# Optimization experiments

Hardware: AMD Instinct MI355X
Metric: run time of the kernel (lower is better)

The kernel has to match this reference:

```python
import jax, jax.numpy as jnp
import numpy as np

N = 100000   # num_nodes
E = 1600000  # num_edges
IN, HID, OUT = 128, 128, 64
BN_EPS = 1e-5


def setup_inputs() -> dict:
    key = jax.random.key(0)
    ks = jax.random.split(key, 8)
    x = jax.random.normal(ks[0], (N, IN), jnp.float32)
    edge_index = jax.random.randint(ks[1], (2, E), 0, N)
    edge_weight = jax.random.uniform(ks[2], (E,), jnp.float32)
    W1 = jax.random.normal(ks[3], (IN, HID), jnp.float32) / np.sqrt(IN)
    b1 = jnp.zeros((HID,), jnp.float32)
    gamma = jnp.ones((HID,), jnp.float32)
    beta = jnp.zeros((HID,), jnp.float32)
    W2 = jax.random.normal(ks[4], (HID, OUT), jnp.float32) / np.sqrt(HID)
    b2 = jnp.zeros((OUT,), jnp.float32)
    return {"x": x, "edge_index": edge_index, "edge_weight": edge_weight,
            "W1": W1, "b1": b1, "gamma": gamma, "beta": beta, "W2": W2, "b2": b2}


def _add_self_loops(edge_index, edge_weight, n):
    loops = jnp.arange(n, dtype=edge_index.dtype)
    row = jnp.concatenate([edge_index[0], loops])
    col = jnp.concatenate([edge_index[1], loops])
    ew = jnp.concatenate([edge_weight, jnp.ones((n,), edge_weight.dtype)])
    return row, col, ew


def _gcn_conv(x, row, col, ew, W, b, n):
    h = x @ W                                           # [n, out]
    deg = jax.ops.segment_sum(ew, col, num_segments=n)  # in-degree (incl. self-loops)
    dinv = jnp.where(deg > 0, jax.lax.rsqrt(jnp.where(deg > 0, deg, 1.0)), 0.0)
    norm = dinv[row] * ew * dinv[col]                   # [E+n]
    msg = h[row] * norm[:, None]                        # gather + scale
    out = jax.ops.segment_sum(msg, col, num_segments=n)  # scatter-add at targets
    return out + b


def reference(x, edge_index, edge_weight, W1, b1, gamma, beta, W2, b2):
    n = x.shape[0]
    row, col, ew = _add_self_loops(edge_index, edge_weight, n)
    h = _gcn_conv(x, row, col, ew, W1, b1, n)
    # BatchNorm1d over nodes (training-mode batch stats, biased variance)
    mu = h.mean(axis=0)
    var = ((h - mu) ** 2).mean(axis=0)
    h = (h - mu) * jax.lax.rsqrt(var + BN_EPS) * gamma + beta
    h = jax.nn.relu(h)
    # dropout is identity at inference
    h = _gcn_conv(h, row, col, ew, W2, b2, n)
    return jax.nn.log_softmax(h, axis=1)  # out_feats > 1 branch
```

## Files before the change

kernel.cpp:

```cpp
#include <hip/hip_runtime.h>
#include <math.h>


typedef unsigned int   uint;
typedef unsigned short ushort;
typedef __bf16 bf16x8 __attribute__((ext_vector_type(8)));
typedef float  f32x4  __attribute__((ext_vector_type(4)));

union U16 { uint4 u; bf16x8 b; };

__device__ __forceinline__ void atomAddF(float* p, float v) {
    __hip_atomic_fetch_add(p, v, __ATOMIC_RELAXED, __HIP_MEMORY_SCOPE_AGENT);
}

__device__ __forceinline__ ushort f2bf(float f) {
    uint u = __float_as_uint(f);
    u += 0x7FFFu + ((u >> 16) & 1u);
    return (ushort)(u >> 16);
}
__device__ __forceinline__ float bf2f(ushort h) {
    return __uint_as_float(((uint)h) << 16);
}
__device__ __forceinline__ uint pack2(float f0, float f1) {
    return (uint)f2bf(f0) | ((uint)f2bf(f1) << 16);
}

__global__ void k_init(int* __restrict__ cnt, float* __restrict__ bn, int n) {
    int i = blockIdx.x * 256 + threadIdx.x;
    if (i < n) cnt[i] = 0;
    if (i < 256) bn[i] = 0.0f;
}

__global__ void k_cnt(const int* __restrict__ col, int* __restrict__ cnt,
                      int* __restrict__ rank, int e) {
    int i = blockIdx.x * 256 + threadIdx.x;
    if (i < e) rank[i] = atomicAdd(&cnt[col[i]], 1);
}


__global__ __launch_bounds__(256)
void k_scanA(const int* __restrict__ cnt, int* __restrict__ bsum, int n) {
    __shared__ int ls[256];
    int base = blockIdx.x * 1024 + threadIdx.x * 4;
    int s = 0;
#pragma unroll
    for (int k = 0; k < 4; ++k) { int i = base + k; if (i < n) s += cnt[i]; }
    ls[threadIdx.x] = s;
    __syncthreads();
    for (int d = 128; d > 0; d >>= 1) {
        if (threadIdx.x < d) ls[threadIdx.x] += ls[threadIdx.x + d];
        __syncthreads();
    }
    if (threadIdx.x == 0) bsum[blockIdx.x] = ls[0];
}

__global__ __launch_bounds__(1024)
void k_scanB(int* __restrict__ bsum, int* __restrict__ ptr, int nblk, int n) {
    __shared__ int ls[1024];
    int t = threadIdx.x;
    int v = (t < nblk) ? bsum[t] : 0;
    ls[t] = v;
    __syncthreads();
    for (int d = 1; d < 1024; d <<= 1) {
        int mine = ls[t];
        int up   = (t >= d) ? ls[t - d] : 0;
        __syncthreads();
        ls[t] = mine + up;
        __syncthreads();
    }
    if (t < nblk) bsum[t] = ls[t] - v;
    if (t == 0) ptr[n] = ls[1023];
}

__global__ __launch_bounds__(256)
void k_scanC(const int* __restrict__ cnt, const int* __restrict__ bsum,
             int* __restrict__ ptr, int n) {
    __shared__ int ls[256];
    int base = blockIdx.x * 1024 + threadIdx.x * 4;
    int v[4];
#pragma unroll
    for (int k = 0; k < 4; ++k) { int i = base + k; v[k] = (i < n) ? cnt[i] : 0; }
    int t = v[0] + v[1] + v[2] + v[3];
    ls[threadIdx.x] = t;
    __syncthreads();
    for (int d = 1; d < 256; d <<= 1) {
        int mine = ls[threadIdx.x];
        int up   = (threadIdx.x >= d) ? ls[threadIdx.x - d] : 0;
        __syncthreads();
        ls[threadIdx.x] = mine + up;
        __syncthreads();
    }
    int off = bsum[blockIdx.x] + ls[threadIdx.x] - t;
    int pf = 0;
#pragma unroll
    for (int k = 0; k < 4; ++k) {
        int i = base + k;
        if (i < n) ptr[i] = off + pf;
        pf += v[k];
    }
}

__global__ void k_fill(const int* __restrict__ row, const int* __restrict__ col,
                       const float* __restrict__ ew, const int* __restrict__ rank,
                       const int* __restrict__ ptr, int2* __restrict__ csr, int e) {
    int i = blockIdx.x * 256 + threadIdx.x;
    if (i < e) {
        int pos = ptr[col[i]] + rank[i];
        int2 pr;
        pr.x = row[i];
        pr.y = __float_as_int(ew[i]);
        csr[pos] = pr;
    }
}

__global__ __launch_bounds__(256)
void k_degsum(const int* __restrict__ ptr, const int2* __restrict__ csr,
              float* __restrict__ dinv, int n) {
    int lane = threadIdx.x & 15;
    int node = (blockIdx.x * 256 + threadIdx.x) >> 4;
    if (node >= n) return;
    int p0 = ptr[node], p1 = ptr[node + 1];
    float s = 0.f;
    for (int j = p0 + lane; j < p1; j += 16) s += __int_as_float(csr[j].y);
#pragma unroll
    for (int off = 8; off > 0; off >>= 1) s += __shfl_xor(s, off, 16);
    if (lane == 0) dinv[node] = rsqrtf(1.0f + s);
}

__global__ void k_wfrag(const float* __restrict__ W, uint4* __restrict__ Wf, int M) {
    int t = blockIdx.x * 256 + threadIdx.x;
    if (t >= M * 16) return;
    int l  = t & 63;
    int ks = (t >> 6) & 3;
    int nt = t >> 8;
    int kbase = ks * 32 + (l >> 4) * 8;
    int colj  = nt * 16 + (l & 15);
    float v[8];
#pragma unroll
    for (int j = 0; j < 8; ++j) v[j] = W[(kbase + j) * M + colj];
    uint4 o;
    o.x = pack2(v[0], v[1]);
    o.y = pack2(v[2], v[3]);
    o.z = pack2(v[4], v[5]);
    o.w = pack2(v[6], v[7]);
    Wf[t] = o;
}

template<int M, bool BN>
__global__ __launch_bounds__(256)
void k_mfma(const void* __restrict__ Xv, const uint4* __restrict__ Wf,
            const float* __restrict__ scale, const float* __restrict__ shift,
            ushort* __restrict__ H, int n)
{
    constexpr int NT = M / 16;
    const int l = threadIdx.x & 63;
    const int w = threadIdx.x >> 6;
    const int rowbase = blockIdx.x * 64 + w * 16;
    const int arow = rowbase + (l & 15);
    const bool rv = arow < n;
    const int koff = (l >> 4) * 8;

    f32x4 acc[NT];
#pragma unroll
    for (int t = 0; t < NT; ++t) acc[t] = (f32x4){0.f, 0.f, 0.f, 0.f};

#pragma unroll
    for (int ks = 0; ks < 4; ++ks) {
        U16 ua;
        if (BN) {
            const ushort* xr = (const ushort*)Xv + (size_t)arow * 128 + koff;
            U16 xa; xa.u = make_uint4(0, 0, 0, 0);
            if (rv) xa.u = *(const uint4*)(xr + ks * 32);
            int k0 = ks * 32 + koff;
            float4 sc0 = *(const float4*)(scale + k0);
            float4 sc1 = *(const float4*)(scale + k0 + 4);
            float4 sh0 = *(const float4*)(shift + k0);
            float4 sh1 = *(const float4*)(shift + k0 + 4);
            float a[8];
            a[0] = fmaxf(0.f, fmaf(bf2f((ushort)(xa.u.x)),       sc0.x, sh0.x));
            a[1] = fmaxf(0.f, fmaf(bf2f((ushort)(xa.u.x >> 16)), sc0.y, sh0.y));
            a[2] = fmaxf(0.f, fmaf(bf2f((ushort)(xa.u.y)),       sc0.z, sh0.z));
            a[3] = fmaxf(0.f, fmaf(bf2f((ushort)(xa.u.y >> 16)), sc0.w, sh0.w));
            a[4] = fmaxf(0.f, fmaf(bf2f((ushort)(xa.u.z)),       sc1.x, sh1.x));
            a[5] = fmaxf(0.f, fmaf(bf2f((ushort)(xa.u.z >> 16)), sc1.y, sh1.y));
            a[6] = fmaxf(0.f, fmaf(bf2f((ushort)(xa.u.w)),       sc1.z, sh1.z));
            a[7] = fmaxf(0.f, fmaf(bf2f((ushort)(xa.u.w >> 16)), sc1.w, sh1.w));
            ua.u.x = pack2(a[0], a[1]);
            ua.u.y = pack2(a[2], a[3]);
            ua.u.z = pack2(a[4], a[5]);
            ua.u.w = pack2(a[6], a[7]);
        } else {
            const float* xr = (const float*)Xv + (size_t)arow * 128 + koff;
            float4 a0 = make_float4(0.f, 0.f, 0.f, 0.f);
            float4 a1 = a0;
            if (rv) {
                a0 = *(const float4*)(xr + ks * 32);
                a1 = *(const float4*)(xr + ks * 32 + 4);
            }
            ua.u.x = pack2(a0.x, a0.y);
            ua.u.y = pack2(a0.z, a0.w);
            ua.u.z = pack2(a1.x, a1.y);
            ua.u.w = pack2(a1.z, a1.w);
        }
#pragma unroll
        for (int nt = 0; nt < NT; ++nt) {
            U16 ub;
            ub.u = Wf[(nt * 4 + ks) * 64 + l];
            acc[nt] = __builtin_amdgcn_mfma_f32_16x16x32_bf16(ua.b, ub.b, acc[nt], 0, 0, 0);
        }
    }

    __shared__ __align__(16) ushort lds[4][16][M + 8];
#pragma unroll
    for (int nt = 0; nt < NT; ++nt)
#pragma unroll
        for (int r = 0; r < 4; ++r)
            lds[w][(l >> 4) * 4 + r][nt * 16 + (l & 15)] = f2bf(acc[nt][r]);
    __syncthreads();

    constexpr int LPR = M / 8;
    constexpr int RPP = 64 / LPR;
#pragma unroll
    for (int it = 0; it < 16 / RPP; ++it) {
        int rl = it * RPP + (l / LPR);
        int gr = rowbase + rl;
        if (gr < n)
            *(uint4*)(H + (size_t)gr * M + (l % LPR) * 8) =
                *(const uint4*)&lds[w][rl][(l % LPR) * 8];
    }
}

__global__ __launch_bounds__(256)
void k_gather1(const int* __restrict__ ptr, const int2* __restrict__ csr,
               const ushort* __restrict__ h, const float* __restrict__ dinv,
               const float* __restrict__ bias, ushort* __restrict__ out, int n)
{
    int lane = threadIdx.x & 15;
    int node = (blockIdx.x * 256 + threadIdx.x) >> 4;
    if (node >= n) return;
    int p0 = ptr[node], p1 = ptr[node + 1];
    float di = dinv[node];
    float s  = di * di;

    U16 hv; hv.u = *(const uint4*)(h + (size_t)node * 128 + lane * 8);
    float4 b0 = *(const float4*)(bias + lane * 8);
    float4 b1v = *(const float4*)(bias + lane * 8 + 4);
    float acc[8];
    acc[0] = fmaf(bf2f((ushort)(hv.u.x)),       s, b0.x);
    acc[1] = fmaf(bf2f((ushort)(hv.u.x >> 16)), s, b0.y);
    acc[2] = fmaf(bf2f((ushort)(hv.u.y)),       s, b0.z);
    acc[3] = fmaf(bf2f((ushort)(hv.u.y >> 16)), s, b0.w);
    acc[4] = fmaf(bf2f((ushort)(hv.u.z)),       s, b1v.x);
    acc[5] = fmaf(bf2f((ushort)(hv.u.z >> 16)), s, b1v.y);
    acc[6] = fmaf(bf2f((ushort)(hv.u.w)),       s, b1v.z);
    acc[7] = fmaf(bf2f((ushort)(hv.u.w >> 16)), s, b1v.w);

#pragma unroll 4
    for (int j = p0; j < p1; ++j) {
        int2 pr = csr[j];
        float w = __int_as_float(pr.y) * di * dinv[pr.x];
        U16 v; v.u = *(const uint4*)(h + (size_t)pr.x * 128 + lane * 8);
        acc[0] = fmaf(bf2f((ushort)(v.u.x)),       w, acc[0]);
        acc[1] = fmaf(bf2f((ushort)(v.u.x >> 16)), w, acc[1]);
        acc[2] = fmaf(bf2f((ushort)(v.u.y)),       w, acc[2]);
        acc[3] = fmaf(bf2f((ushort)(v.u.y >> 16)), w, acc[3]);
        acc[4] = fmaf(bf2f((ushort)(v.u.z)),       w, acc[4]);
        acc[5] = fmaf(bf2f((ushort)(v.u.z >> 16)), w, acc[5]);
        acc[6] = fmaf(bf2f((ushort)(v.u.w)),       w, acc[6]);
        acc[7] = fmaf(bf2f((ushort)(v.u.w >> 16)), w, acc[7]);
    }

    U16 o;
    o.u.x = pack2(acc[0], acc[1]);
    o.u.y = pack2(acc[2], acc[3]);
    o.u.z = pack2(acc[4], acc[5]);
    o.u.w = pack2(acc[6], acc[7]);
    *(uint4*)(out + (size_t)node * 128 + lane * 8) = o.u;
}

__global__ __launch_bounds__(256)
void k_gather2(const int* __restrict__ ptr, const int2* __restrict__ csr,
               const ushort* __restrict__ h, const float* __restrict__ dinv,
               const float* __restrict__ bias, float* __restrict__ out, int n)
{
    int lane = threadIdx.x & 7;
    int node = (blockIdx.x * 256 + threadIdx.x) >> 3;
    if (node >= n) return;
    int p0 = ptr[node], p1 = ptr[node + 1];
    float di = dinv[node];
    float s  = di * di;

    U16 hv; hv.u = *(const uint4*)(h + (size_t)node * 64 + lane * 8);
    float4 b0 = *(const float4*)(bias + lane * 8);
    float4 b1v = *(const float4*)(bias + lane * 8 + 4);
    float acc[8];
    acc[0] = fmaf(bf2f((ushort)(hv.u.x)),       s, b0.x);
    acc[1] = fmaf(bf2f((ushort)(hv.u.x >> 16)), s, b0.y);
    acc[2] = fmaf(bf2f((ushort)(hv.u.y)),       s, b0.z);
    acc[3] = fmaf(bf2f((ushort)(hv.u.y >> 16)), s, b0.w);
    acc[4] = fmaf(bf2f((ushort)(hv.u.z)),       s, b1v.x);
    acc[5] = fmaf(bf2f((ushort)(hv.u.z >> 16)), s, b1v.y);
    acc[6] = fmaf(bf2f((ushort)(hv.u.w)),       s, b1v.z);
    acc[7] = fmaf(bf2f((ushort)(hv.u.w >> 16)), s, b1v.w);

#pragma unroll 4
    for (int j = p0; j < p1; ++j) {
        int2 pr = csr[j];
        float w = __int_as_float(pr.y) * di * dinv[pr.x];
        U16 v; v.u = *(const uint4*)(h + (size_t)pr.x * 64 + lane * 8);
        acc[0] = fmaf(bf2f((ushort)(v.u.x)),       w, acc[0]);
        acc[1] = fmaf(bf2f((ushort)(v.u.x >> 16)), w, acc[1]);
        acc[2] = fmaf(bf2f((ushort)(v.u.y)),       w, acc[2]);
        acc[3] = fmaf(bf2f((ushort)(v.u.y >> 16)), w, acc[3]);
        acc[4] = fmaf(bf2f((ushort)(v.u.z)),       w, acc[4]);
        acc[5] = fmaf(bf2f((ushort)(v.u.z >> 16)), w, acc[5]);
        acc[6] = fmaf(bf2f((ushort)(v.u.w)),       w, acc[6]);
        acc[7] = fmaf(bf2f((ushort)(v.u.w >> 16)), w, acc[7]);
    }

    float m = acc[0];
#pragma unroll
    for (int k = 1; k < 8; ++k) m = fmaxf(m, acc[k]);
#pragma unroll
    for (int off = 1; off < 8; off <<= 1) m = fmaxf(m, __shfl_xor(m, off, 64));
    float sum = 0.f;
#pragma unroll
    for (int k = 0; k < 8; ++k) sum += expf(acc[k] - m);
#pragma unroll
    for (int off = 1; off < 8; off <<= 1) sum += __shfl_xor(sum, off, 64);
    float lse = m + logf(sum);

    float* orow = out + (size_t)node * 64 + lane * 8;
    *(float4*)(orow)     = make_float4(acc[0] - lse, acc[1] - lse, acc[2] - lse, acc[3] - lse);
    *(float4*)(orow + 4) = make_float4(acc[4] - lse, acc[5] - lse, acc[6] - lse, acc[7] - lse);
}

__global__ __launch_bounds__(256)
void k_bn_stats(const ushort* __restrict__ a, float* __restrict__ sums,
                float* __restrict__ sumsq, int n)
{
    int fp = threadIdx.x & 63;
    int rg = threadIdx.x >> 6;
    float s0 = 0.f, q0 = 0.f, s1 = 0.f, q1 = 0.f;
    for (int r = blockIdx.x * 4 + rg; r < n; r += gridDim.x * 4) {
        uint v = *(const uint*)(a + (size_t)r * 128 + fp * 2);
        float x0 = bf2f((ushort)v), x1 = bf2f((ushort)(v >> 16));
        s0 += x0; q0 += x0 * x0;
        s1 += x1; q1 += x1 * x1;
    }
    __shared__ float l0[256], l1[256], l2[256], l3[256];
    l0[threadIdx.x] = s0; l1[threadIdx.x] = q0;
    l2[threadIdx.x] = s1; l3[threadIdx.x] = q1;
    __syncthreads();
    if (rg == 0) {
        float S0 = l0[fp] + l0[fp + 64] + l0[fp + 128] + l0[fp + 192];
        float Q0 = l1[fp] + l1[fp + 64] + l1[fp + 128] + l1[fp + 192];
        float S1 = l2[fp] + l2[fp + 64] + l2[fp + 128] + l2[fp + 192];
        float Q1 = l3[fp] + l3[fp + 64] + l3[fp + 128] + l3[fp + 192];
        atomAddF(&sums[fp * 2],     S0);
        atomAddF(&sumsq[fp * 2],    Q0);
        atomAddF(&sums[fp * 2 + 1], S1);
        atomAddF(&sumsq[fp * 2 + 1], Q1);
    }
}

__global__ void k_bn_final(const float* __restrict__ bn, const float* __restrict__ gamma,
                           const float* __restrict__ beta, float* __restrict__ scale,
                           float* __restrict__ shift, int n)
{
    int f = threadIdx.x;
    if (f < 128) {
        float inv_n = 1.0f / (float)n;
        float mu  = bn[f] * inv_n;
        float var = bn[128 + f] * inv_n - mu * mu;
        float rstd = rsqrtf(var + 1e-5f);
        float sc = gamma[f] * rstd;
        scale[f] = sc;
        shift[f] = beta[f] - mu * sc;
    }
}

extern "C" void kernel_launch(void* const* d_in, const int* in_sizes, int n_in,
                              void* d_out, int out_size, void* d_ws, size_t ws_size,
                              hipStream_t stream)
{
    const float* x     = (const float*)d_in[0];
    const int*   ei    = (const int*)  d_in[1];
    const float* ew    = (const float*)d_in[2];
    const float* W1    = (const float*)d_in[3];
    const float* b1    = (const float*)d_in[4];
    const float* gamma = (const float*)d_in[5];
    const float* beta  = (const float*)d_in[6];
    const float* W2    = (const float*)d_in[7];
    const float* b2    = (const float*)d_in[8];

    const int n = in_sizes[0] / 128;
    const int e = in_sizes[2];
    const int* row = ei;
    const int* col = ei + e;

    float* ws    = (float*)d_ws;
    size_t off   = 0;
    float* dinv  = ws + off; off += n;
    ushort* h1   = (ushort*)(ws + off); off += (size_t)n * 64;
    ushort* agg1 = (ushort*)(ws + off); off += (size_t)n * 64;
    float* bn    = ws + off; off += 256;
    float* scale = ws + off; off += 128;
    float* shift = ws + off; off += 128;
    int*   cnt   = (int*)(ws + off); off += n;
    int*   ptr   = (int*)(ws + off); off += (size_t)(n + 1);
    int*   bsum  = (int*)(ws + off); off += 1024;
    off = (off + 3) & ~(size_t)3;
    uint4* w1f   = (uint4*)(ws + off); off += 8192;
    uint4* w2f   = (uint4*)(ws + off); off += 4096;
    int2*  csr   = (int2*)(ws + off);
    int*   rank  = (int*)agg1;
    ushort* h2   = h1;
    float* outp  = (float*)d_out;

    const int nb_n = (n + 255) / 256;
    const int nb_e = (e + 255) / 256;
    const int nb_qpn = (n + 15) / 16;
    const int nb_opn = (n + 31) / 32;
    const int nb_mf  = (n + 63) / 64;
    const int nblk_scan = (n + 1023) / 1024;

    k_wfrag<<<8, 256, 0, stream>>>(W1, w1f, 128);
    k_wfrag<<<4, 256, 0, stream>>>(W2, w2f, 64);

    k_init<<<nb_n, 256, 0, stream>>>(cnt, bn, n);
    k_cnt<<<nb_e, 256, 0, stream>>>(col, cnt, rank, e);
    k_scanA<<<nblk_scan, 256, 0, stream>>>(cnt, bsum, n);
    k_scanB<<<1, 1024, 0, stream>>>(bsum, ptr, nblk_scan, n);
    k_scanC<<<nblk_scan, 256, 0, stream>>>(cnt, bsum, ptr, n);
    k_fill<<<nb_e, 256, 0, stream>>>(row, col, ew, rank, ptr, csr, e);
    k_degsum<<<nb_qpn, 256, 0, stream>>>(ptr, csr, dinv, n);

    k_mfma<128, false><<<nb_mf, 256, 0, stream>>>(x, w1f, nullptr, nullptr, h1, n);
    k_gather1<<<nb_qpn, 256, 0, stream>>>(ptr, csr, h1, dinv, b1, agg1, n);

    k_bn_stats<<<256, 256, 0, stream>>>(agg1, bn, bn + 128, n);
    k_bn_final<<<1, 128, 0, stream>>>(bn, gamma, beta, scale, shift, n);

    k_mfma<64, true><<<nb_mf, 256, 0, stream>>>(agg1, w2f, scale, shift, h2, n);
    k_gather2<<<nb_opn, 256, 0, stream>>>(ptr, csr, h2, dinv, b2, outp, n);
}
```

Baseline: 290.0 us.

## Split per-node edge counters into eight sub-counters to reduce atomic contention

Each node's in-degree counter becomes eight sub-counters, chosen by the low bits of the edge index, so atomic increments on a popular target node are spread out. The scan now runs over n*8 interleaved entries, producing a bucketed CSR pointer array that fill, degsum and the gather kernels index with node<<3. The rank buffer moves to its own workspace region instead of aliasing agg1. In exchange the count/scan arrays are eight times larger, and the scan kernels read them with a strided pattern.

```diff
diff --git a/kernel.cpp b/kernel.cpp
--- a/kernel.cpp
+++ b/kernel.cpp
@@ -25,26 +25,30 @@
     return (uint)f2bf(f0) | ((uint)f2bf(f1) << 16);
 }
 
-__global__ void k_init(int* __restrict__ cnt, float* __restrict__ bn, int n) {
+__global__ void k_init(int* __restrict__ cnt, float* __restrict__ bn, int m) {
     int i = blockIdx.x * 256 + threadIdx.x;
-    if (i < n) cnt[i] = 0;
+    if (i < m) cnt[i] = 0;
     if (i < 256) bn[i] = 0.0f;
 }
 
 __global__ void k_cnt(const int* __restrict__ col, int* __restrict__ cnt,
-                      int* __restrict__ rank, int e) {
+                      int* __restrict__ rank, int e, int n) {
     int i = blockIdx.x * 256 + threadIdx.x;
-    if (i < e) rank[i] = atomicAdd(&cnt[col[i]], 1);
-}
-
-
-__global__ __launch_bounds__(256)
-void k_scanA(const int* __restrict__ cnt, int* __restrict__ bsum, int n) {
+    if (i < e) rank[i] = atomicAdd(&cnt[(i & 7) * n + col[i]], 1);
+}
+
+
+__global__ __launch_bounds__(256)
+void k_scanA(const int* __restrict__ cnt, int* __restrict__ bsum,
+             int m, int n) {
     __shared__ int ls[256];
     int base = blockIdx.x * 1024 + threadIdx.x * 4;
     int s = 0;
 #pragma unroll
-    for (int k = 0; k < 4; ++k) { int i = base + k; if (i < n) s += cnt[i]; }
+    for (int k = 0; k < 4; ++k) {
+        int b = base + k;
+        if (b < m) s += cnt[(b & 7) * n + (b >> 3)];
+    }
     ls[threadIdx.x] = s;
     __syncthreads();
     for (int d = 128; d > 0; d >>= 1) {
@@ -55,7 +59,7 @@
 }
 
 __global__ __launch_bounds__(1024)
-void k_scanB(int* __restrict__ bsum, int* __restrict__ ptr, int nblk, int n) {
+void k_scanB(int* __restrict__ bsum, int* __restrict__ ptr, int nblk, int m) {
     __shared__ int ls[1024];
     int t = threadIdx.x;
     int v = (t < nblk) ? bsum[t] : 0;
@@ -69,17 +73,20 @@
         __syncthreads();
     }
     if (t < nblk) bsum[t] = ls[t] - v;
-    if (t == 0) ptr[n] = ls[1023];
+    if (t == 0) ptr[m] = ls[1023];
 }
 
 __global__ __launch_bounds__(256)
 void k_scanC(const int* __restrict__ cnt, const int* __restrict__ bsum,
-             int* __restrict__ ptr, int n) {
+             int* __restrict__ ptr, int m, int n) {
     __shared__ int ls[256];
     int base = blockIdx.x * 1024 + threadIdx.x * 4;
     int v[4];
 #pragma unroll
-    for (int k = 0; k < 4; ++k) { int i = base + k; v[k] = (i < n) ? cnt[i] : 0; }
+    for (int k = 0; k < 4; ++k) {
+        int b = base + k;
+        v[k] = (b < m) ? cnt[(b & 7) * n + (b >> 3)] : 0;
+    }
     int t = v[0] + v[1] + v[2] + v[3];
     ls[threadIdx.x] = t;
     __syncthreads();
@@ -94,8 +101,8 @@
     int pf = 0;
 #pragma unroll
     for (int k = 0; k < 4; ++k) {
-        int i = base + k;
-        if (i < n) ptr[i] = off + pf;
+        int b = base + k;
+        if (b < m) ptr[b] = off + pf;
         pf += v[k];
     }
 }
@@ -105,7 +112,7 @@
                        const int* __restrict__ ptr, int2* __restrict__ csr, int e) {
     int i = blockIdx.x * 256 + threadIdx.x;
     if (i < e) {
-        int pos = ptr[col[i]] + rank[i];
+        int pos = ptr[(col[i] << 3) + (i & 7)] + rank[i];
         int2 pr;
         pr.x = row[i];
         pr.y = __float_as_int(ew[i]);
@@ -119,7 +126,7 @@
     int lane = threadIdx.x & 15;
     int node = (blockIdx.x * 256 + threadIdx.x) >> 4;
     if (node >= n) return;
-    int p0 = ptr[node], p1 = ptr[node + 1];
+    int p0 = ptr[node << 3], p1 = ptr[(node << 3) + 8];
     float s = 0.f;
     for (int j = p0 + lane; j < p1; j += 16) s += __int_as_float(csr[j].y);
 #pragma unroll
@@ -238,7 +245,7 @@
     int lane = threadIdx.x & 15;
     int node = (blockIdx.x * 256 + threadIdx.x) >> 4;
     if (node >= n) return;
-    int p0 = ptr[node], p1 = ptr[node + 1];
+    int p0 = ptr[node << 3], p1 = ptr[(node << 3) + 8];
     float di = dinv[node];
     float s  = di * di;
 
@@ -286,7 +293,7 @@
     int lane = threadIdx.x & 7;
     int node = (blockIdx.x * 256 + threadIdx.x) >> 3;
     if (node >= n) return;
-    int p0 = ptr[node], p1 = ptr[node + 1];
+    int p0 = ptr[node << 3], p1 = ptr[(node << 3) + 8];
     float di = dinv[node];
     float s  = di * di;
 
@@ -357,9 +364,9 @@
         float Q0 = l1[fp] + l1[fp + 64] + l1[fp + 128] + l1[fp + 192];
         float S1 = l2[fp] + l2[fp + 64] + l2[fp + 128] + l2[fp + 192];
         float Q1 = l3[fp] + l3[fp + 64] + l3[fp + 128] + l3[fp + 192];
-        atomAddF(&sums[fp * 2],     S0);
-        atomAddF(&sumsq[fp * 2],    Q0);
-        atomAddF(&sums[fp * 2 + 1], S1);
+        atomAddF(&sums[fp * 2],      S0);
+        atomAddF(&sumsq[fp * 2],     Q0);
+        atomAddF(&sums[fp * 2 + 1],  S1);
         atomAddF(&sumsq[fp * 2 + 1], Q1);
     }
 }
@@ -398,6 +405,7 @@
     const int e = in_sizes[2];
     const int* row = ei;
     const int* col = ei + e;
+    const int m = n * 8;
 
     float* ws    = (float*)d_ws;
     size_t off   = 0;
@@ -407,32 +415,32 @@
     float* bn    = ws + off; off += 256;
     float* scale = ws + off; off += 128;
     float* shift = ws + off; off += 128;
-    int*   cnt   = (int*)(ws + off); off += n;
-    int*   ptr   = (int*)(ws + off); off += (size_t)(n + 1);
+    int*   cnt   = (int*)(ws + off); off += (size_t)m;
+    int*   ptr   = (int*)(ws + off); off += (size_t)(m + 1);
     int*   bsum  = (int*)(ws + off); off += 1024;
     off = (off + 3) & ~(size_t)3;
     uint4* w1f   = (uint4*)(ws + off); off += 8192;
     uint4* w2f   = (uint4*)(ws + off); off += 4096;
-    int2*  csr   = (int2*)(ws + off);
-    int*   rank  = (int*)agg1;
+    int2*  csr   = (int2*)(ws + off); off += (size_t)e * 2;
+    int*   rank  = (int*)(ws + off);
     ushort* h2   = h1;
     float* outp  = (float*)d_out;
 
-    const int nb_n = (n + 255) / 256;
+    const int nb_m = (m + 255) / 256;
     const int nb_e = (e + 255) / 256;
     const int nb_qpn = (n + 15) / 16;
     const int nb_opn = (n + 31) / 32;
     const int nb_mf  = (n + 63) / 64;
-    const int nblk_scan = (n + 1023) / 1024;
+    const int nblk_scan = (m + 1023) / 1024;
 
     k_wfrag<<<8, 256, 0, stream>>>(W1, w1f, 128);
     k_wfrag<<<4, 256, 0, stream>>>(W2, w2f, 64);
 
-    k_init<<<nb_n, 256, 0, stream>>>(cnt, bn, n);
-    k_cnt<<<nb_e, 256, 0, stream>>>(col, cnt, rank, e);
-    k_scanA<<<nblk_scan, 256, 0, stream>>>(cnt, bsum, n);
-    k_scanB<<<1, 1024, 0, stream>>>(bsum, ptr, nblk_scan, n);
-    k_scanC<<<nblk_scan, 256, 0, stream>>>(cnt, bsum, ptr, n);
+    k_init<<<nb_m, 256, 0, stream>>>(cnt, bn, m);
+    k_cnt<<<nb_e, 256, 0, stream>>>(col, cnt, rank, e, n);
+    k_scanA<<<nblk_scan, 256, 0, stream>>>(cnt, bsum, m, n);
+    k_scanB<<<1, 1024, 0, stream>>>(bsum, ptr, nblk_scan, m);
+    k_scanC<<<nblk_scan, 256, 0, stream>>>(cnt, bsum, ptr, m, n);
     k_fill<<<nb_e, 256, 0, stream>>>(row, col, ew, rank, ptr, csr, e);
     k_degsum<<<nb_qpn, 256, 0, stream>>>(ptr, csr, dinv, n);
 
```

After: 301.7 us. 1.04x slower.

## Build CSR via two-level bucketed counting sort with shared-memory atomics

Applied to the files above, without the earlier changes.

Replaces the global-atomic per-edge counting sort with a two-pass radix-style partition. Edges are first histogrammed into 512-node buckets per edge chunk in shared memory, then scattered into bucket order. A per-bucket kernel builds local CSR offsets, the degree sums and dinv using shared-memory atomics, so the separate degree-sum kernel goes away. It aims to remove contended global atomics and random scatter writes, at the cost of an extra edge buffer pass and more workspace.

```diff
diff --git a/kernel.cpp b/kernel.cpp
--- a/kernel.cpp
+++ b/kernel.cpp
@@ -7,6 +7,9 @@
 typedef __bf16 bf16x8 __attribute__((ext_vector_type(8)));
 typedef float  f32x4  __attribute__((ext_vector_type(4)));
 
+#define EPB  4096
+#define BSH  9
+
 union U16 { uint4 u; bf16x8 b; };
 
 __device__ __forceinline__ void atomAddF(float* p, float v) {
@@ -25,26 +28,27 @@
     return (uint)f2bf(f0) | ((uint)f2bf(f1) << 16);
 }
 
-__global__ void k_init(int* __restrict__ cnt, float* __restrict__ bn, int n) {
-    int i = blockIdx.x * 256 + threadIdx.x;
-    if (i < n) cnt[i] = 0;
-    if (i < 256) bn[i] = 0.0f;
-}
-
-__global__ void k_cnt(const int* __restrict__ col, int* __restrict__ cnt,
-                      int* __restrict__ rank, int e) {
-    int i = blockIdx.x * 256 + threadIdx.x;
-    if (i < e) rank[i] = atomicAdd(&cnt[col[i]], 1);
-}
-
-
-__global__ __launch_bounds__(256)
-void k_scanA(const int* __restrict__ cnt, int* __restrict__ bsum, int n) {
+__global__ __launch_bounds__(256)
+void k_p1(const int* __restrict__ col, int* __restrict__ ghist,
+          int e, int PB) {
+    __shared__ int lh[256];
+    lh[threadIdx.x] = 0;
+    __syncthreads();
+    int base = blockIdx.x * EPB;
+    int end  = base + EPB; if (end > e) end = e;
+    for (int j = base + threadIdx.x; j < end; j += 256)
+        atomicAdd(&lh[col[j] >> BSH], 1);
+    __syncthreads();
+    ghist[threadIdx.x * PB + blockIdx.x] = lh[threadIdx.x];
+}
+
+__global__ __launch_bounds__(256)
+void k_scanA(const int* __restrict__ v, int* __restrict__ bsum, int tot) {
     __shared__ int ls[256];
     int base = blockIdx.x * 1024 + threadIdx.x * 4;
     int s = 0;
 #pragma unroll
-    for (int k = 0; k < 4; ++k) { int i = base + k; if (i < n) s += cnt[i]; }
+    for (int k = 0; k < 4; ++k) { int i = base + k; if (i < tot) s += v[i]; }
     ls[threadIdx.x] = s;
     __syncthreads();
     for (int d = 128; d > 0; d >>= 1) {
@@ -55,9 +59,10 @@
 }
 
 __global__ __launch_bounds__(1024)
-void k_scanB(int* __restrict__ bsum, int* __restrict__ ptr, int nblk, int n) {
+void k_scanB(int* __restrict__ bsum, float* __restrict__ bn, int nblk) {
     __shared__ int ls[1024];
     int t = threadIdx.x;
+    if (t < 256) bn[t] = 0.0f;
     int v = (t < nblk) ? bsum[t] : 0;
     ls[t] = v;
     __syncthreads();
@@ -69,18 +74,17 @@
         __syncthreads();
     }
     if (t < nblk) bsum[t] = ls[t] - v;
-    if (t == 0) ptr[n] = ls[1023];
-}
-
-__global__ __launch_bounds__(256)
-void k_scanC(const int* __restrict__ cnt, const int* __restrict__ bsum,
-             int* __restrict__ ptr, int n) {
+}
+
+__global__ __launch_bounds__(256)
+void k_scanC(const int* __restrict__ v, const int* __restrict__ bsum,
+             int* __restrict__ gout, int tot) {
     __shared__ int ls[256];
     int base = blockIdx.x * 1024 + threadIdx.x * 4;
-    int v[4];
-#pragma unroll
-    for (int k = 0; k < 4; ++k) { int i = base + k; v[k] = (i < n) ? cnt[i] : 0; }
-    int t = v[0] + v[1] + v[2] + v[3];
+    int w[4];
+#pragma unroll
+    for (int k = 0; k < 4; ++k) { int i = base + k; w[k] = (i < tot) ? v[i] : 0; }
+    int t = w[0] + w[1] + w[2] + w[3];
     ls[threadIdx.x] = t;
     __syncthreads();
     for (int d = 1; d < 256; d <<= 1) {
@@ -95,36 +99,82 @@
 #pragma unroll
     for (int k = 0; k < 4; ++k) {
         int i = base + k;
-        if (i < n) ptr[i] = off + pf;
-        pf += v[k];
-    }
-}
-
-__global__ void k_fill(const int* __restrict__ row, const int* __restrict__ col,
-                       const float* __restrict__ ew, const int* __restrict__ rank,
-                       const int* __restrict__ ptr, int2* __restrict__ csr, int e) {
-    int i = blockIdx.x * 256 + threadIdx.x;
-    if (i < e) {
-        int pos = ptr[col[i]] + rank[i];
-        int2 pr;
-        pr.x = row[i];
-        pr.y = __float_as_int(ew[i]);
-        csr[pos] = pr;
-    }
-}
-
-__global__ __launch_bounds__(256)
-void k_degsum(const int* __restrict__ ptr, const int2* __restrict__ csr,
-              float* __restrict__ dinv, int n) {
-    int lane = threadIdx.x & 15;
-    int node = (blockIdx.x * 256 + threadIdx.x) >> 4;
-    if (node >= n) return;
-    int p0 = ptr[node], p1 = ptr[node + 1];
-    float s = 0.f;
-    for (int j = p0 + lane; j < p1; j += 16) s += __int_as_float(csr[j].y);
-#pragma unroll
-    for (int off = 8; off > 0; off >>= 1) s += __shfl_xor(s, off, 16);
-    if (lane == 0) dinv[node] = rsqrtf(1.0f + s);
+        if (i < tot) gout[i] = off + pf;
+        pf += w[k];
+    }
+}
+
+__global__ __launch_bounds__(256)
+void k_p3(const int* __restrict__ row, const int* __restrict__ col,
+          const float* __restrict__ ew, const int* __restrict__ goff,
+          int2* __restrict__ ebuf, ushort* __restrict__ ecol,
+          int e, int PB) {
+    __shared__ int cur[256];
+    cur[threadIdx.x] = 0;
+    __syncthreads();
+    int blk  = blockIdx.x;
+    int base = blk * EPB;
+    int end  = base + EPB; if (end > e) end = e;
+    for (int j = base + threadIdx.x; j < end; j += 256) {
+        int c = col[j];
+        int b = c >> BSH;
+        int r = atomicAdd(&cur[b], 1);
+        int pos = goff[b * PB + blk] + r;
+        ebuf[pos] = make_int2(row[j], __float_as_int(ew[j]));
+        ecol[pos] = (ushort)(c & ((1 << BSH) - 1));
+    }
+}
+
+__global__ __launch_bounds__(512)
+void k_p4(const int* __restrict__ goff, const int2* __restrict__ ebuf,
+          const ushort* __restrict__ ecol, int2* __restrict__ csr,
+          int* __restrict__ ptr, float* __restrict__ dinv,
+          int n, int e, int PB, int NB) {
+    __shared__ int   cnt[512];
+    __shared__ float fs[512];
+    __shared__ int   cur2[512];
+    __shared__ int   sc[512];
+    int tid = threadIdx.x;
+    int b   = blockIdx.x;
+    int bstart = goff[b * PB];
+    int bend   = (b == NB - 1) ? e : goff[(b + 1) * PB];
+
+    cnt[tid] = 0; fs[tid] = 0.f; cur2[tid] = 0;
+    __syncthreads();
+
+    for (int j = bstart + tid; j < bend; j += 512) {
+        int c = (int)ecol[j];
+        atomicAdd(&cnt[c], 1);
+        atomicAdd(&fs[c], __int_as_float(ebuf[j].y));
+    }
+    __syncthreads();
+
+    int v = cnt[tid];
+    sc[tid] = v;
+    __syncthreads();
+    for (int d = 1; d < 512; d <<= 1) {
+        int mine = sc[tid];
+        int up   = (tid >= d) ? sc[tid - d] : 0;
+        __syncthreads();
+        sc[tid] = mine + up;
+        __syncthreads();
+    }
+    int excl = sc[tid] - v;
+
+    int node = (b << BSH) + tid;
+    if (node < n) {
+        ptr[node]  = bstart + excl;
+        dinv[node] = rsqrtf(1.0f + fs[tid]);
+    }
+    cnt[tid] = excl;
+    __syncthreads();
+
+    for (int j = bstart + tid; j < bend; j += 512) {
+        int c = (int)ecol[j];
+        int r = atomicAdd(&cur2[c], 1);
+        csr[bstart + cnt[c] + r] = ebuf[j];
+    }
+    if (b == 0 && tid == 0) ptr[n] = e;
 }
 
 __global__ void k_wfrag(const float* __restrict__ W, uint4* __restrict__ Wf, int M) {
@@ -357,9 +407,9 @@
         float Q0 = l1[fp] + l1[fp + 64] + l1[fp + 128] + l1[fp + 192];
         float S1 = l2[fp] + l2[fp + 64] + l2[fp + 128] + l2[fp + 192];
         float Q1 = l3[fp] + l3[fp + 64] + l3[fp + 128] + l3[fp + 192];
-        atomAddF(&sums[fp * 2],     S0);
-        atomAddF(&sumsq[fp * 2],    Q0);
-        atomAddF(&sums[fp * 2 + 1], S1);
+        atomAddF(&sums[fp * 2],      S0);
+        atomAddF(&sumsq[fp * 2],     Q0);
+        atomAddF(&sums[fp * 2 + 1],  S1);
         atomAddF(&sumsq[fp * 2 + 1], Q1);
     }
 }
@@ -399,6 +449,10 @@
     const int* row = ei;
     const int* col = ei + e;
 
+    const int PB  = (e + EPB - 1) / EPB;
+    const int NB  = (n + (1 << BSH) - 1) >> BSH;
+    const int tot = NB * PB;
+
     float* ws    = (float*)d_ws;
     size_t off   = 0;
     float* dinv  = ws + off; off += n;
@@ -407,34 +461,33 @@
     float* bn    = ws + off; off += 256;
     float* scale = ws + off; off += 128;
     float* shift = ws + off; off += 128;
-    int*   cnt   = (int*)(ws + off); off += n;
     int*   ptr   = (int*)(ws + off); off += (size_t)(n + 1);
     int*   bsum  = (int*)(ws + off); off += 1024;
+    int*   ghist = (int*)(ws + off); off += (size_t)PB * 256;
+    int*   goff  = (int*)(ws + off); off += (size_t)(tot + 1);
     off = (off + 3) & ~(size_t)3;
     uint4* w1f   = (uint4*)(ws + off); off += 8192;
     uint4* w2f   = (uint4*)(ws + off); off += 4096;
-    int2*  csr   = (int2*)(ws + off);
-    int*   rank  = (int*)agg1;
+    int2*  ebuf  = (int2*)(ws + off); off += (size_t)e * 2;
+    int2*  csr   = (int2*)(ws + off); off += (size_t)e * 2;
+    ushort* ecol = (ushort*)(ws + off); off += (size_t)(e + 1) / 2;
     ushort* h2   = h1;
     float* outp  = (float*)d_out;
 
-    const int nb_n = (n + 255) / 256;
-    const int nb_e = (e + 255) / 256;
     const int nb_qpn = (n + 15) / 16;
     const int nb_opn = (n + 31) / 32;
     const int nb_mf  = (n + 63) / 64;
-    const int nblk_scan = (n + 1023) / 1024;
+    const int nblk_scan = (tot + 1023) / 1024;
 
     k_wfrag<<<8, 256, 0, stream>>>(W1, w1f, 128);
     k_wfrag<<<4, 256, 0, stream>>>(W2, w2f, 64);
 
-    k_init<<<nb_n, 256, 0, stream>>>(cnt, bn, n);
-    k_cnt<<<nb_e, 256, 0, stream>>>(col, cnt, rank, e);
-    k_scanA<<<nblk_scan, 256, 0, stream>>>(cnt, bsum, n);
-    k_scanB<<<1, 1024, 0, stream>>>(bsum, ptr, nblk_scan, n);
-    k_scanC<<<nblk_scan, 256, 0, stream>>>(cnt, bsum, ptr, n);
-    k_fill<<<nb_e, 256, 0, stream>>>(row, col, ew, rank, ptr, csr, e);
-    k_degsum<<<nb_qpn, 256, 0, stream>>>(ptr, csr, dinv, n);
+    k_p1<<<PB, 256, 0, stream>>>(col, ghist, e, PB);
+    k_scanA<<<nblk_scan, 256, 0, stream>>>(ghist, bsum, tot);
+    k_scanB<<<1, 1024, 0, stream>>>(bsum, bn, nblk_scan);
+    k_scanC<<<nblk_scan, 256, 0, stream>>>(ghist, bsum, goff, tot);
+    k_p3<<<PB, 256, 0, stream>>>(row, col, ew, goff, ebuf, ecol, e, PB);
+    k_p4<<<NB, 512, 0, stream>>>(goff, ebuf, ecol, csr, ptr, dinv, n, e, PB, NB);
 
     k_mfma<128, false><<<nb_mf, 256, 0, stream>>>(x, w1f, nullptr, nullptr, h1, n);
     k_gather1<<<nb_qpn, 256, 0, stream>>>(ptr, csr, h1, dinv, b1, agg1, n);
```

Measured after the change: 253.0 us. 1.15x faster.
